# Performance work log

Hardware: AMD Instinct MI355X
Metric: run time of the kernel (lower is better)

Reference implementation:

```python
import jax, jax.numpy as jnp
import numpy as np

B, T, V, H = 64, 1024, 512, 512


def setup_inputs() -> dict:
    key = jax.random.key(0)
    ks = jax.random.split(key, 10)
    s = 0.01
    return {
        "X": jax.random.normal(ks[0], (B, T, V), dtype=jnp.float32),
        "state": jnp.zeros((B, H), dtype=jnp.float32),
        "candidate": jnp.zeros((B, H), dtype=jnp.float32),
        "w_xf": jax.random.normal(ks[1], (V, H), dtype=jnp.float32) * s,
        "w_hf": jax.random.normal(ks[2], (H, H), dtype=jnp.float32) * s,
        "b_f": jnp.zeros((H,), dtype=jnp.float32),
        "w_xi": jax.random.normal(ks[3], (V, H), dtype=jnp.float32) * s,
        "w_hi": jax.random.normal(ks[4], (H, H), dtype=jnp.float32) * s,
        "b_i": jnp.zeros((H,), dtype=jnp.float32),
        "w_xo": jax.random.normal(ks[5], (V, H), dtype=jnp.float32) * s,
        "w_ho": jax.random.normal(ks[6], (H, H), dtype=jnp.float32) * s,
        "b_o": jnp.zeros((H,), dtype=jnp.float32),
        "w_xc": jax.random.normal(ks[7], (V, H), dtype=jnp.float32) * s,
        "w_hc": jax.random.normal(ks[8], (H, H), dtype=jnp.float32) * s,
        "b_c": jnp.zeros((H,), dtype=jnp.float32),
        "w_hy": jax.random.normal(ks[9], (H, V), dtype=jnp.float32) * s,
        "b_y": jnp.zeros((V,), dtype=jnp.float32),
    }


def reference(X, state, candidate, w_xf, w_hf, b_f, w_xi, w_hi, b_i,
              w_xo, w_ho, b_o, w_xc, w_hc, b_c, w_hy, b_y):
    # Precompute input projections for all timesteps (same math as per-step mm).
    # Shapes: [T, B, H] (time-major for scan).
    xf = jnp.einsum('btv,vh->tbh', X, w_xf) + b_f
    xi = jnp.einsum('btv,vh->tbh', X, w_xi) + b_i
    xo = jnp.einsum('btv,vh->tbh', X, w_xo) + b_o
    xc = jnp.einsum('btv,vh->tbh', X, w_xc) + b_c

    def step(carry, gates):
        h, c = carry
        gf, gi, go, gc = gates
        f = jax.nn.sigmoid(gf + h @ w_hf)
        i = jax.nn.sigmoid(gi + h @ w_hi)
        o = jax.nn.sigmoid(go + h @ w_ho)
        c_hat = jnp.tanh(gc + h @ w_hc)
        c = f * c + i * c_hat
        h = o * jnp.tanh(c)
        y = h @ w_hy + b_y
        return (h, c), y

    (h_final, c_final), ys = jax.lax.scan(step, (state, candidate), (xf, xi, xo, xc))
    # torch.cat(outputs, dim=0) stacks timesteps along batch dim -> [T*B, V]
    outputs = ys.reshape(T * B, V)
    return outputs, h_final, c_final
```

## Files before the change

### kernel.cpp

```cpp
#include <hip/hip_runtime.h>
#include <hip/hip_bf16.h>
#include <stdint.h>

#define T_STEPS 1024
#define BATCH 64
#define HID 512
#define VOC 512
#define TBV (T_STEPS*BATCH*VOC)
#define POISON 0x7FC17FC1u

typedef __attribute__((ext_vector_type(8))) short bf16x8;
typedef __attribute__((ext_vector_type(8))) unsigned short u16x8;
typedef __attribute__((ext_vector_type(4))) float f32x4;
typedef __attribute__((ext_vector_type(4))) unsigned u32x4;

__device__ __forceinline__ float bf2f(unsigned short u){
  union { unsigned i; float f; } x; x.i = ((unsigned)u)<<16; return x.f;
}
__device__ __forceinline__ unsigned short f2bf(float f){
  union { float f; unsigned i; } x; x.f = f;
  unsigned r = (x.i + 0x7fffu + ((x.i>>16)&1u))>>16;
  return (unsigned short)r;
}
__device__ __forceinline__ float sigm(float x){ return 1.0f/(1.0f+__expf(-x)); }
__device__ __forceinline__ float tanhfast(float x){
  float e = __expf(2.0f*x); return 1.0f - 2.0f/(e+1.0f);
}

__global__ __launch_bounds__(256) void k_pack_x(const float* __restrict__ X,
                                                unsigned short* __restrict__ Xb){
  int idx = blockIdx.x*256 + threadIdx.x;
  int m = idx >> 6, c = idx & 63;
  int b = m & 63, t = m >> 6;
  const float* src = X + ((size_t)b*T_STEPS + t)*VOC + c*8;
  u16x8 v;
  #pragma unroll
  for (int j=0;j<8;j++) v[j] = f2bf(src[j]);
  *(u16x8*)(Xb + (size_t)m*VOC + c*8) = v;
}

__global__ __launch_bounds__(256) void k_pack_wx(const float* __restrict__ wf,
                                                 const float* __restrict__ wi,
                                                 const float* __restrict__ wo,
                                                 const float* __restrict__ wc,
                                                 unsigned short* __restrict__ Wx4t){
  int idx = blockIdx.x*256 + threadIdx.x;
  int n = idx >> 6, c = idx & 63;
  const float* w = (n<512)?wf:(n<1024)?wi:(n<1536)?wo:wc;
  int h = n & 511;
  u16x8 v;
  #pragma unroll
  for (int j=0;j<8;j++) v[j] = f2bf(w[(size_t)(c*8+j)*HID + h]);
  *(u16x8*)(Wx4t + (size_t)n*HID + c*8) = v;
}

__global__ __launch_bounds__(256) void k_pack_wh(const float* __restrict__ whf,
                                                 const float* __restrict__ whi,
                                                 const float* __restrict__ who,
                                                 const float* __restrict__ whc,
                                                 const float* __restrict__ why,
                                                 unsigned short* __restrict__ Wt){
  int idx = blockIdx.x*256 + threadIdx.x;
  int mat = idx >> 15;
  int rem = idx & 32767;
  int col = rem >> 6, c = rem & 63;
  const float* w = (mat==0)?whf:(mat==1)?whi:(mat==2)?who:(mat==3)?whc:why;
  u16x8 v;
  #pragma unroll
  for (int j=0;j<8;j++) v[j] = f2bf(w[(size_t)(c*8+j)*HID + col]);
  *(u16x8*)(Wt + ((size_t)mat*HID + col)*HID + c*8) = v;
}

__global__ __launch_bounds__(256) void k_poison(unsigned* __restrict__ ring){
  size_t i = ((size_t)blockIdx.x*256 + threadIdx.x)*16;
  u32x4 v = {POISON, POISON, POISON, POISON};
  asm volatile("global_store_dwordx4 %0, %1, off sc0 sc1"
               :: "v"((char*)ring + i), "v"(v) : "memory");
}

__global__ __launch_bounds__(256) void k_init_h(const float* __restrict__ state,
                                                unsigned short* __restrict__ ring){
  int idx = blockIdx.x*256 + threadIdx.x;
  int row = idx >> 6, col8 = idx & 63;
  int gt = col8 >> 1, hf = col8 & 1;
  const float* src = state + (size_t)row*HID + col8*8;
  union { unsigned short us[8]; u32x4 v; } u;
  #pragma unroll
  for (int j=0;j<8;j++) u.us[j] = f2bf(src[j]);
  char* dst = (char*)ring + (((size_t)gt*64 + row)*16 + hf*8)*2;
  asm volatile("global_store_dwordx4 %0, %1, off sc0 sc1"
               :: "v"(dst), "v"(u.v) : "memory");
}

__global__ __launch_bounds__(256) void k_gemm_xg(const unsigned short* __restrict__ Xb,
                                                 const unsigned short* __restrict__ Wx4t,
                                                 unsigned short* __restrict__ XG){
  __shared__ unsigned short Al[128*64];
  __shared__ unsigned short Bl[128*64];
  int tid = threadIdx.x;
  int bid = blockIdx.x;
  int bn = bid & 15, bm = bid >> 4;
  int lane = tid & 63, w = tid >> 6;
  int wm = w >> 1, wn = w & 1;
  int l15 = lane & 15, l4 = lane >> 4;

  f32x4 zero = {0.f,0.f,0.f,0.f};
  f32x4 acc[4][4];
  #pragma unroll
  for (int mi=0;mi<4;mi++)
    #pragma unroll
    for (int ni=0;ni<4;ni++) acc[mi][ni] = zero;

  for (int bk=0; bk<8; ++bk){
    if (bk) __syncthreads();
    #pragma unroll
    for (int it=0; it<4; ++it){
      int L = it*4096 + tid*16;
      int r = L >> 7, ow = L & 127;
      int sw = ow ^ ((r&7)<<4);
      u16x8 va = *(const u16x8*)((const char*)Xb   + (size_t)(bm*128 + r)*1024 + bk*128 + ow);
      u16x8 vb = *(const u16x8*)((const char*)Wx4t + (size_t)(bn*128 + r)*1024 + bk*128 + ow);
      *(u16x8*)((char*)Al + r*128 + sw) = va;
      *(u16x8*)((char*)Bl + r*128 + sw) = vb;
    }
    __syncthreads();
    #pragma unroll
    for (int kt=0; kt<2; ++kt){
      int kb = kt*64 + 16*l4;
      bf16x8 af[4], bfr[4];
      #pragma unroll
      for (int mi=0;mi<4;mi++){
        int r = wm*64 + mi*16 + l15;
        af[mi] = *(const bf16x8*)((const char*)Al + r*128 + (kb ^ ((r&7)<<4)));
      }
      #pragma unroll
      for (int ni=0;ni<4;ni++){
        int r = wn*64 + ni*16 + l15;
        bfr[ni] = *(const bf16x8*)((const char*)Bl + r*128 + (kb ^ ((r&7)<<4)));
      }
      #pragma unroll
      for (int mi=0;mi<4;mi++)
        #pragma unroll
        for (int ni=0;ni<4;ni++)
          acc[mi][ni] = __builtin_amdgcn_mfma_f32_16x16x32_bf16(af[mi], bfr[ni], acc[mi][ni], 0,0,0);
    }
  }
  #pragma unroll
  for (int mi=0;mi<4;mi++){
    int rowb = bm*128 + wm*64 + mi*16 + l4*4;
    #pragma unroll
    for (int ni=0;ni<4;ni++){
      int col = bn*128 + wn*64 + ni*16 + l15;
      #pragma unroll
      for (int r=0;r<4;r++)
        XG[(size_t)(rowb+r)*2048 + col] = f2bf(acc[mi][ni][r]);
    }
  }
}

__global__ __launch_bounds__(320) void k_scan(
  const unsigned short* __restrict__ XG, const unsigned short* __restrict__ Wt,
  unsigned short* __restrict__ ring,
  const float* __restrict__ cand,
  const float* __restrict__ b_f, const float* __restrict__ b_i,
  const float* __restrict__ b_o, const float* __restrict__ b_c,
  const float* __restrict__ b_y,
  float* __restrict__ out)
{
  __shared__ char h_lds[16*1024];
  __shared__ float gate_lds[4][16][20];
  int tid = threadIdx.x;
  int w = tid >> 6, lane = tid & 63;
  int l15 = lane & 15, l4 = lane >> 4;
  int grp = blockIdx.x >> 5, g = blockIdx.x & 31;
  int colbase = g*16, rowbase = grp*16;

  u32x4 breg[16];
  {
    const char* wb = (const char*)Wt + ((size_t)(w*HID + colbase + l15))*HID*2 + l4*16;
    #pragma unroll
    for (int kt=0; kt<16; ++kt)
      asm volatile("global_load_dwordx4 %0, %1, off" : "=v"(breg[kt]) : "v"(wb + kt*64));
    asm volatile("s_waitcnt vmcnt(0)" ::: "memory");
    __builtin_amdgcn_sched_barrier(0);
  }

  int cr = tid >> 4, cc = tid & 15;
  int colg = colbase + cc, browg = rowbase + cr;
  float c_val = 0.f, bfv=0.f, biv=0.f, bov=0.f, bcv=0.f;
  if (tid < 256){
    c_val = cand[(size_t)browg*HID + colg];
    bfv = b_f[colg]; biv = b_i[colg]; bov = b_o[colg]; bcv = b_c[colg];
  }
  float byv = (w==4) ? b_y[colbase + l15] : 0.f;

  int rr = (tid>>1) & 15, hf = tid & 1;
  int g0 = tid >> 5;
  int off32[4], ldsw[4]; bool ownj[4];
  #pragma unroll
  for (int j=0;j<4;j++){
    int gj = g0 + 8*j;
    off32[j] = gj*2048 + (rowbase+rr)*32 + hf*16;
    ldsw[j]  = rr*1024 + ((gj*32 + hf*16) ^ ((rr&7)<<4));
    ownj[j]  = (gj == g);
  }

  for (int t=0; t<=T_STEPS; ++t){
    float xf_r=0.f, xi_r=0.f, xo_r=0.f, xc_r=0.f;
    if (t < T_STEPS && tid < 256){
      const unsigned short* xg = XG + ((size_t)t*64 + browg)*2048 + colg;
      xf_r = bf2f(xg[0]);    xi_r = bf2f(xg[512]);
      xo_r = bf2f(xg[1024]); xc_r = bf2f(xg[1536]);
    }
    const char* rt = (const char*)ring + (size_t)t*65536;
    if (tid < 256){
      const char* p0 = rt + off32[0];
      const char* p1 = rt + off32[1];
      const char* p2 = rt + off32[2];
      const char* p3 = rt + off32[3];
      u32x4 h0, h1, h2, h3;
      for (;;){
        asm volatile(
          "global_load_dwordx4 %0, %4, off sc0 sc1\n\t"
          "global_load_dwordx4 %1, %5, off sc0 sc1\n\t"
          "global_load_dwordx4 %2, %6, off sc0 sc1\n\t"
          "global_load_dwordx4 %3, %7, off sc0 sc1\n\t"
          "s_waitcnt vmcnt(0)"
          : "=&v"(h0), "=&v"(h1), "=&v"(h2), "=&v"(h3)
          : "v"(p0), "v"(p1), "v"(p2), "v"(p3)
          : "memory");
        bool ok = true;
        if (!(ownj[0] && t>0)) ok &= (h0[0]!=POISON)&(h0[1]!=POISON)&(h0[2]!=POISON)&(h0[3]!=POISON);
        if (!(ownj[1] && t>0)) ok &= (h1[0]!=POISON)&(h1[1]!=POISON)&(h1[2]!=POISON)&(h1[3]!=POISON);
        if (!(ownj[2] && t>0)) ok &= (h2[0]!=POISON)&(h2[1]!=POISON)&(h2[2]!=POISON)&(h2[3]!=POISON);
        if (!(ownj[3] && t>0)) ok &= (h3[0]!=POISON)&(h3[1]!=POISON)&(h3[2]!=POISON)&(h3[3]!=POISON);
        if (ok) break;
        __builtin_amdgcn_s_sleep(1);
      }
      if (!(ownj[0] && t>0)) *(u32x4*)(h_lds + ldsw[0]) = h0;
      if (!(ownj[1] && t>0)) *(u32x4*)(h_lds + ldsw[1]) = h1;
      if (!(ownj[2] && t>0)) *(u32x4*)(h_lds + ldsw[2]) = h2;
      if (!(ownj[3] && t>0)) *(u32x4*)(h_lds + ldsw[3]) = h3;
    }
    __syncthreads();

    f32x4 acc0 = {0.f,0.f,0.f,0.f}, acc1 = {0.f,0.f,0.f,0.f};
    #pragma unroll
    for (int kt=0; kt<16; kt+=2){
      bf16x8 a0 = *(const bf16x8*)(h_lds + l15*1024 + (((kt  )*64 + l4*16) ^ ((l15&7)<<4)));
      bf16x8 a1 = *(const bf16x8*)(h_lds + l15*1024 + (((kt+1)*64 + l4*16) ^ ((l15&7)<<4)));
      acc0 = __builtin_amdgcn_mfma_f32_16x16x32_bf16(a0, __builtin_bit_cast(bf16x8, breg[kt]),   acc0, 0,0,0);
      acc1 = __builtin_amdgcn_mfma_f32_16x16x32_bf16(a1, __builtin_bit_cast(bf16x8, breg[kt+1]), acc1, 0,0,0);
    }
    f32x4 accv = acc0 + acc1;

    if (w < 4){
      if (t < T_STEPS){
        #pragma unroll
        for (int r=0;r<4;r++) gate_lds[w][l4*4+r][l15] = accv[r];
      }
    } else if (t >= 1){
      #pragma unroll
      for (int r=0;r<4;r++)
        out[((size_t)(t-1)*64 + rowbase + l4*4 + r)*VOC + colbase + l15] = accv[r] + byv;
    }
    __syncthreads();

    if (t < T_STEPS && tid < 256){
      float gf = xf_r + bfv + gate_lds[0][cr][cc];
      float gi = xi_r + biv + gate_lds[1][cr][cc];
      float go = xo_r + bov + gate_lds[2][cr][cc];
      float gc = xc_r + bcv + gate_lds[3][cr][cc];
      float fv = sigm(gf), iv = sigm(gi), ov = sigm(go);
      c_val = fv*c_val + iv*tanhfast(gc);
      float hvf = ov*tanhfast(c_val);
      unsigned hb16 = f2bf(hvf);
      *(unsigned short*)(h_lds + cr*1024 + ((g*32 + cc*2) ^ ((cr&7)<<4))) = (unsigned short)hb16;
      char* hp = (char*)ring + (size_t)(t+1)*65536 + g*2048 + (rowbase+cr)*32 + cc*2;
      asm volatile("global_store_short %0, %1, off sc0 sc1"
                   :: "v"(hp), "v"(hb16) : "memory");
      if (t == T_STEPS-1){
        out[(size_t)TBV + (size_t)browg*512 + colg] = hvf;
        out[(size_t)TBV + 32768 + (size_t)browg*512 + colg] = c_val;
      }
    }
  }
}

extern "C" void kernel_launch(void* const* d_in, const int* in_sizes, int n_in,
                              void* d_out, int out_size, void* d_ws, size_t ws_size,
                              hipStream_t stream){
  const float* X    = (const float*)d_in[0];
  const float* state= (const float*)d_in[1];
  const float* cand = (const float*)d_in[2];
  const float* w_xf = (const float*)d_in[3];
  const float* w_hf = (const float*)d_in[4];
  const float* b_f  = (const float*)d_in[5];
  const float* w_xi = (const float*)d_in[6];
  const float* w_hi = (const float*)d_in[7];
  const float* b_i  = (const float*)d_in[8];
  const float* w_xo = (const float*)d_in[9];
  const float* w_ho = (const float*)d_in[10];
  const float* b_o  = (const float*)d_in[11];
  const float* w_xc = (const float*)d_in[12];
  const float* w_hc = (const float*)d_in[13];
  const float* b_c  = (const float*)d_in[14];
  const float* w_hy = (const float*)d_in[15];
  const float* b_y  = (const float*)d_in[16];
  float* out = (float*)d_out;

  char* ws = (char*)d_ws;
  unsigned short* XG   = (unsigned short*)(ws);
  unsigned short* Xb   = (unsigned short*)(ws + 268435456);
  unsigned short* ring = (unsigned short*)(ws + 268435456);
  unsigned short* Wx4t = (unsigned short*)(ws + 335609856);
  unsigned short* Wt   = (unsigned short*)(ws + 337707008);

  k_pack_x <<<16384,256,0,stream>>>(X, Xb);
  k_pack_wx<<<  512,256,0,stream>>>(w_xf,w_xi,w_xo,w_xc, Wx4t);
  k_pack_wh<<<  640,256,0,stream>>>(w_hf,w_hi,w_ho,w_hc,w_hy, Wt);
  k_gemm_xg<<< 8192,256,0,stream>>>(Xb, Wx4t, XG);
  k_poison <<<16400,256,0,stream>>>((unsigned*)ring);
  k_init_h <<<   16,256,0,stream>>>(state, ring);
  k_scan   <<<  128,320,0,stream>>>(XG, Wt, ring, cand, b_f,b_i,b_o,b_c,b_y, out);
}
```

Before: 2.210 ms.

## Tile XG per scan block and prefetch next-step gate inputs

```diff
diff --git a/kernel.cpp b/kernel.cpp
--- a/kernel.cpp
+++ b/kernel.cpp
@@ -13,6 +13,7 @@
 typedef __attribute__((ext_vector_type(8))) unsigned short u16x8;
 typedef __attribute__((ext_vector_type(4))) float f32x4;
 typedef __attribute__((ext_vector_type(4))) unsigned u32x4;
+typedef __attribute__((ext_vector_type(2))) unsigned u32x2;
 
 __device__ __forceinline__ float bf2f(unsigned short u){
   union { unsigned i; float f; } x; x.i = ((unsigned)u)<<16; return x.f;
@@ -94,7 +95,7 @@
 
 __global__ __launch_bounds__(256) void k_gemm_xg(const unsigned short* __restrict__ Xb,
                                                  const unsigned short* __restrict__ Wx4t,
-                                                 unsigned short* __restrict__ XG){
+                                                 unsigned short* __restrict__ XG2){
   __shared__ unsigned short Al[128*64];
   __shared__ unsigned short Bl[128*64];
   int tid = threadIdx.x;
@@ -145,21 +146,23 @@
           acc[mi][ni] = __builtin_amdgcn_mfma_f32_16x16x32_bf16(af[mi], bfr[ni], acc[mi][ni], 0,0,0);
     }
   }
+  int t0 = bm*2 + wm;
   #pragma unroll
   for (int mi=0;mi<4;mi++){
-    int rowb = bm*128 + wm*64 + mi*16 + l4*4;
     #pragma unroll
     for (int ni=0;ni<4;ni++){
-      int col = bn*128 + wn*64 + ni*16 + l15;
-      #pragma unroll
-      for (int r=0;r<4;r++)
-        XG[(size_t)(rowb+r)*2048 + col] = f2bf(acc[mi][ni][r]);
+      int col = bn*128 + wn*64 + ni*16;
+      int gate = col >> 9, gg = (col >> 4) & 31;
+      size_t base = (((size_t)t0*4 + mi)*32 + gg)*1024 + (size_t)gate*256 + l15;
+      #pragma unroll
+      for (int rr=0;rr<4;rr++)
+        XG2[base + (size_t)(l4*4+rr)*16] = f2bf(acc[mi][ni][rr]);
     }
   }
 }
 
 __global__ __launch_bounds__(320) void k_scan(
-  const unsigned short* __restrict__ XG, const unsigned short* __restrict__ Wt,
+  const unsigned short* __restrict__ XG2, const unsigned short* __restrict__ Wt,
   unsigned short* __restrict__ ring,
   const float* __restrict__ cand,
   const float* __restrict__ b_f, const float* __restrict__ b_i,
@@ -205,13 +208,13 @@
     ownj[j]  = (gj == g);
   }
 
+  unsigned short xgf=0, xgi=0, xgo=0, xgc=0;
+  if (tid < 256){
+    const unsigned short* x0 = XG2 + ((size_t)grp*32 + g)*1024;
+    xgf = x0[tid]; xgi = x0[256+tid]; xgo = x0[512+tid]; xgc = x0[768+tid];
+  }
+
   for (int t=0; t<=T_STEPS; ++t){
-    float xf_r=0.f, xi_r=0.f, xo_r=0.f, xc_r=0.f;
-    if (t < T_STEPS && tid < 256){
-      const unsigned short* xg = XG + ((size_t)t*64 + browg)*2048 + colg;
-      xf_r = bf2f(xg[0]);    xi_r = bf2f(xg[512]);
-      xo_r = bf2f(xg[1024]); xc_r = bf2f(xg[1536]);
-    }
     const char* rt = (const char*)ring + (size_t)t*65536;
     if (tid < 256){
       const char* p0 = rt + off32[0];
@@ -244,6 +247,12 @@
     }
     __syncthreads();
 
+    unsigned short xfn=xgf, xin=xgi, xon=xgo, xcn=xgc;
+    if (t+1 < T_STEPS && tid < 256){
+      const unsigned short* xn = XG2 + (((size_t)(t+1)*4 + grp)*32 + g)*1024;
+      xfn = xn[tid]; xin = xn[256+tid]; xon = xn[512+tid]; xcn = xn[768+tid];
+    }
+
     f32x4 acc0 = {0.f,0.f,0.f,0.f}, acc1 = {0.f,0.f,0.f,0.f};
     #pragma unroll
     for (int kt=0; kt<16; kt+=2){
@@ -267,10 +276,10 @@
     __syncthreads();
 
     if (t < T_STEPS && tid < 256){
-      float gf = xf_r + bfv + gate_lds[0][cr][cc];
-      float gi = xi_r + biv + gate_lds[1][cr][cc];
-      float go = xo_r + bov + gate_lds[2][cr][cc];
-      float gc = xc_r + bcv + gate_lds[3][cr][cc];
+      float gf = bf2f(xgf) + bfv + gate_lds[0][cr][cc];
+      float gi = bf2f(xgi) + biv + gate_lds[1][cr][cc];
+      float go = bf2f(xgo) + bov + gate_lds[2][cr][cc];
+      float gc = bf2f(xgc) + bcv + gate_lds[3][cr][cc];
       float fv = sigm(gf), iv = sigm(gi), ov = sigm(go);
       c_val = fv*c_val + iv*tanhfast(gc);
       float hvf = ov*tanhfast(c_val);
@@ -284,6 +293,7 @@
         out[(size_t)TBV + 32768 + (size_t)browg*512 + colg] = c_val;
       }
     }
+    xgf = xfn; xgi = xin; xgo = xon; xgc = xcn;
   }
 }
 
@@ -310,7 +320,7 @@
   float* out = (float*)d_out;
 
   char* ws = (char*)d_ws;
-  unsigned short* XG   = (unsigned short*)(ws);
+  unsigned short* XG2  = (unsigned short*)(ws);
   unsigned short* Xb   = (unsigned short*)(ws + 268435456);
   unsigned short* ring = (unsigned short*)(ws + 268435456);
   unsigned short* Wx4t = (unsigned short*)(ws + 335609856);
@@ -319,8 +329,8 @@
   k_pack_x <<<16384,256,0,stream>>>(X, Xb);
   k_pack_wx<<<  512,256,0,stream>>>(w_xf,w_xi,w_xo,w_xc, Wx4t);
   k_pack_wh<<<  640,256,0,stream>>>(w_hf,w_hi,w_ho,w_hc,w_hy, Wt);
-  k_gemm_xg<<< 8192,256,0,stream>>>(Xb, Wx4t, XG);
+  k_gemm_xg<<< 8192,256,0,stream>>>(Xb, Wx4t, XG2);
   k_poison <<<16400,256,0,stream>>>((unsigned*)ring);
   k_init_h <<<   16,256,0,stream>>>(state, ring);
-  k_scan   <<<  128,320,0,stream>>>(XG, Wt, ring, cand, b_f,b_i,b_o,b_c,b_y, out);
-}
+  k_scan   <<<  128,320,0,stream>>>(XG2, Wt, ring, cand, b_f,b_i,b_o,b_c,b_y, out);
+}
```

After: 2.157 ms. -2.4%, faster.
